# Kernel tuning notes

Measured on AMD Instinct MI355X. Metric: run time of the kernel, lower is better.

## Reference

```python
import jax, jax.numpy as jnp
import numpy as np

TT_IN = (8, 8, 8, 8)
TT_OUT = (8, 8, 8, 8)
TT_RANKS = (1, 32, 32, 32, 1)
BATCH = 4096
N_IN = int(np.prod(TT_IN))     # 4096
N_OUT = int(np.prod(TT_OUT))   # 4096
KERNEL_LEN = int(sum(TT_RANKS[k] * TT_IN[k] * TT_OUT[k] * TT_RANKS[k + 1]
                     for k in range(len(TT_IN))))  # 135168


def setup_inputs() -> dict:
    key = jax.random.key(0)
    kx, kk = jax.random.split(key)
    x = jax.random.normal(kx, (BATCH, N_IN), dtype=jnp.float32)
    # flat packed TT cores (the layer stores all cores in one 1-D weight)
    kernel = 0.02 * jax.random.normal(kk, (KERNEL_LEN,), dtype=jnp.float32)
    bias = jnp.zeros((N_OUT,), dtype=jnp.float32)
    return {"x": x, "kernel": kernel, "bias": bias}


def reference(x, kernel, bias):
    # Faithful translation of TensorTrainDense.call: iterate cores k = d-1 .. 0,
    # slicing the flat kernel from index 0 (matching the original code exactly).
    batch = x.shape[0]
    res = x
    idx = 0
    for k in range(len(TT_IN) - 1, -1, -1):
        m = TT_IN[k] * TT_RANKS[k + 1]   # contraction dim
        n = TT_RANKS[k] * TT_OUT[k]      # output dim of this core
        core = kernel[idx:idx + m * n].reshape(m, n)
        res = res.reshape(-1, m) @ core              # (-1, r_k*out_k)
        res = res.reshape(-1, TT_OUT[k]).T           # (out_k, -1)
        idx += m * n
    res = res.reshape(-1, batch).T                   # (batch, prod(out))
    return res + bias
```

## Files before the change

### kernel.cpp

```cpp
#include <hip/hip_runtime.h>
#include <hip/hip_bf16.h>

typedef unsigned short u16;
typedef __attribute__((ext_vector_type(8))) short  bf16x8;
typedef __attribute__((ext_vector_type(4))) float  fx4;

#define OFF_C0 0
#define OFF_C1 2048
#define OFF_C2 67584
#define OFF_C3 133120

static __device__ __forceinline__ u16 f2bf(float f) {
  union { __hip_bfloat16 h; u16 u; } cv;
  cv.h = __float2bfloat16(f);
  return cv.u;
}
static __device__ __forceinline__ float bf2f(u16 u) {
  union { u16 u; __hip_bfloat16 h; } cv;
  cv.u = u;
  return __bfloat162float(cv.h);
}

__global__ void build_w34T(const float* __restrict__ ker, float* __restrict__ w34T) {
  int t = blockIdx.x * 256 + threadIdx.x;
  int i34 = t & 63, c = t >> 6;
  int a2 = c >> 6, o3 = (c >> 3) & 7, o4 = c & 7;
  int i3 = i34 >> 3, i4 = i34 & 7;
  float s = 0.f;
#pragma unroll 8
  for (int a3 = 0; a3 < 32; ++a3) {
    float k1 = ker[OFF_C1 + (i3 * 32 + a3) * 256 + a2 * 8 + o3];
    float k0 = ker[OFF_C0 + i4 * 256 + a3 * 8 + o4];
    s += k1 * k0;
  }
  w34T[c * 64 + i34] = s;
}

__global__ void build_w234t2(const float* __restrict__ ker, const float* __restrict__ w34T,
                             u16* __restrict__ w234t) {
  int t = blockIdx.x * 256 + threadIdx.x;
  int i234 = t & 511, g = t >> 9;
  int a1 = g >> 3, o3 = g & 7;
  int i2 = i234 >> 6, i34 = i234 & 63;
  float acc[8][8];
#pragma unroll
  for (int a = 0; a < 8; ++a)
#pragma unroll
    for (int b = 0; b < 8; ++b) acc[a][b] = 0.f;
  for (int a2 = 0; a2 < 32; ++a2) {
    float w[8];
#pragma unroll
    for (int o4 = 0; o4 < 8; ++o4)
      w[o4] = w34T[(a2 * 64 + o3 * 8 + o4) * 64 + i34];
#pragma unroll
    for (int o2 = 0; o2 < 8; ++o2) {
      float c2 = ker[OFF_C2 + (i2 * 32 + a2) * 256 + a1 * 8 + o2];
#pragma unroll
      for (int o4 = 0; o4 < 8; ++o4) acc[o2][o4] += c2 * w[o4];
    }
  }
#pragma unroll
  for (int o2 = 0; o2 < 8; ++o2) {
    int cg = a1 * 64 + o2 * 8 + o3;
#pragma unroll
    for (int o4 = 0; o4 < 8; ++o4)
      w234t[(cg * 8 + o4) * 512 + i234] = f2bf(acc[o2][o4]);
  }
}

__global__ void build_wt2(const float* __restrict__ ker, const u16* __restrict__ w234t,
                          u16* __restrict__ wt) {
  int t = blockIdx.x * 256 + threadIdx.x;
  int i234 = t & 511, j234 = t >> 9;
  float acc[8][8];
#pragma unroll
  for (int a = 0; a < 8; ++a)
#pragma unroll
    for (int b = 0; b < 8; ++b) acc[a][b] = 0.f;
  for (int a1 = 0; a1 < 32; ++a1) {
    float w = bf2f(w234t[(a1 * 512 + j234) * 512 + i234]);
#pragma unroll
    for (int i1 = 0; i1 < 8; ++i1) {
      const float* c3 = ker + OFF_C3 + (i1 * 32 + a1) * 8;
#pragma unroll
      for (int o1 = 0; o1 < 8; ++o1) acc[i1][o1] += c3[o1] * w;
    }
  }
#pragma unroll
  for (int o1 = 0; o1 < 8; ++o1)
#pragma unroll
    for (int i1 = 0; i1 < 8; ++i1)
      wt[(size_t)(o1 * 512 + j234) * 4096 + i1 * 512 + i234] = f2bf(acc[i1][o1]);
}

__global__ void x_to_bf16(const float* __restrict__ x, u16* __restrict__ xb) {
  int t = blockIdx.x * 256 + threadIdx.x;
  const fx4* p = (const fx4*)(x + (size_t)t * 8);
  fx4 v0 = p[0], v1 = p[1];
  u16 tmp[8];
#pragma unroll
  for (int q = 0; q < 4; ++q) tmp[q] = f2bf(v0[q]);
#pragma unroll
  for (int q = 0; q < 4; ++q) tmp[4 + q] = f2bf(v1[q]);
  typedef __attribute__((ext_vector_type(8))) u16 u16x8;
  *(u16x8*)(xb + (size_t)t * 8) = *(const u16x8*)tmp;
}

__device__ __forceinline__ void gld16(const u16* g, u16* l) {
  __builtin_amdgcn_global_load_lds((const __attribute__((address_space(1))) void*)g,
                                   (__attribute__((address_space(3))) void*)l, 16, 0, 0);
}

__global__ __launch_bounds__(512, 2) void gemm_bt4(const u16* __restrict__ A, const u16* __restrict__ Bt,
                                                   const float* __restrict__ bias, float* __restrict__ C) {
  __shared__ __align__(16) u16 sh[65536];

  const int tid = threadIdx.x;
  const int lane = tid & 63;
  const int wave = tid >> 6;
  const int wm = wave >> 2, wn = wave & 3;
  const int fr = lane & 15, fg = lane >> 4;

  const int bid = blockIdx.x;
  const int wg = (bid & 7) * 32 + (bid >> 3);
  const int bm = (wg >> 4) * 256, bn = (wg & 15) * 256;

  const int srow = tid >> 2;
  const int sco = (((tid & 3) ^ ((tid >> 3) & 3)) * 8);
  const size_t agA0 = (size_t)(bm + srow) * 4096 + sco;
  const size_t agA1 = agA0 + (size_t)128 * 4096;
  const size_t agB0 = (size_t)(bn + srow) * 4096 + sco;
  const size_t agB1 = agB0 + (size_t)128 * 4096;
  const int ldsW = wave * 512;

  fx4 acc[8][4];
#pragma unroll
  for (int m = 0; m < 8; ++m)
#pragma unroll
    for (int n = 0; n < 4; ++n) acc[m][n] = (fx4){0.f, 0.f, 0.f, 0.f};

  for (int pt = 0; pt < 3; ++pt) {
    u16* Aq = sh + pt * 8192;
    u16* Bq = sh + 32768 + pt * 8192;
    gld16(A + agA0 + pt * 32, Aq + ldsW);
    gld16(A + agA1 + pt * 32, Aq + ldsW + 4096);
    gld16(Bt + agB0 + pt * 32, Bq + ldsW);
    gld16(Bt + agB1 + pt * 32, Bq + ldsW + 4096);
  }
  asm volatile("s_waitcnt vmcnt(8)" ::: "memory");
  __builtin_amdgcn_s_barrier();

  for (int t = 0; t < 128; ++t) {
    u16* Ap = sh + (t & 3) * 8192;
    u16* Bp = sh + 32768 + (t & 3) * 8192;
    u16* Aq = sh + ((t + 3) & 3) * 8192;
    u16* Bq = sh + 32768 + ((t + 3) & 3) * 8192;
    const size_t ko = (size_t)(((t + 3) & 127) * 32);

    bf16x8 av[4], bv[4], aw[4];
#pragma unroll
    for (int m = 0; m < 4; ++m) {
      const int R = wm * 128 + m * 16 + fr;
      av[m] = *(const bf16x8*)(Ap + R * 32 + ((fg ^ ((R >> 1) & 3)) * 8));
    }
#pragma unroll
    for (int n = 0; n < 4; ++n) {
      const int R = wn * 64 + n * 16 + fr;
      bv[n] = *(const bf16x8*)(Bp + R * 32 + ((fg ^ ((R >> 1) & 3)) * 8));
    }
#pragma unroll
    for (int m = 0; m < 4; ++m) {
      const int R = wm * 128 + 64 + m * 16 + fr;
      aw[m] = *(const bf16x8*)(Ap + R * 32 + ((fg ^ ((R >> 1) & 3)) * 8));
    }

    gld16(A + agA0 + ko, Aq + ldsW);
    gld16(A + agA1 + ko, Aq + ldsW + 4096);
    gld16(Bt + agB0 + ko, Bq + ldsW);
    gld16(Bt + agB1 + ko, Bq + ldsW + 4096);

    __builtin_amdgcn_s_setprio(1);
#pragma unroll
    for (int m = 0; m < 4; ++m)
#pragma unroll
      for (int n = 0; n < 4; ++n)
        acc[m][n] = __builtin_amdgcn_mfma_f32_16x16x32_bf16(av[m], bv[n], acc[m][n], 0, 0, 0);
#pragma unroll
    for (int m = 0; m < 4; ++m)
#pragma unroll
      for (int n = 0; n < 4; ++n)
        acc[4 + m][n] = __builtin_amdgcn_mfma_f32_16x16x32_bf16(aw[m], bv[n], acc[4 + m][n], 0, 0, 0);
    __builtin_amdgcn_s_setprio(0);

    asm volatile("s_waitcnt vmcnt(8)" ::: "memory");
    __builtin_amdgcn_s_barrier();
  }

  const int crow0 = bm + wm * 128 + fg * 4;
  const int ccol0 = bn + wn * 64 + fr;
#pragma unroll
  for (int n = 0; n < 4; ++n) {
    const int col = ccol0 + n * 16;
    const float bvl = bias[col];
#pragma unroll
    for (int mf = 0; mf < 8; ++mf) {
      const int r0 = crow0 + mf * 16;
#pragma unroll
      for (int q = 0; q < 4; ++q)
        C[(size_t)(r0 + q) * 4096 + col] = acc[mf][n][q] + bvl;
    }
  }
}

extern "C" void kernel_launch(void* const* d_in, const int* in_sizes, int n_in,
                              void* d_out, int out_size, void* d_ws, size_t ws_size,
                              hipStream_t stream) {
  const float* x    = (const float*)d_in[0];
  const float* ker  = (const float*)d_in[1];
  const float* bias = (const float*)d_in[2];
  float* out = (float*)d_out;

  char* ws = (char*)d_ws;
  u16*  xb    = (u16*)ws;
  u16*  wt    = (u16*)(ws + 33554432);
  u16*  w234t = (u16*)(ws + 67108864);
  float* w34T = (float*)(ws + 83886080);

  x_to_bf16   <<<8192, 256, 0, stream>>>(x, xb);
  build_w34T  <<<512, 256, 0, stream>>>(ker, w34T);
  build_w234t2<<<512, 256, 0, stream>>>(ker, w34T, w234t);
  build_wt2   <<<1024, 256, 0, stream>>>(ker, w234t, wt);
  gemm_bt4    <<<256, 512, 0, stream>>>(xb, wt, bias, out);
}
```

Measured before the change: 177.5 us.

## Fuse x conversion with w34T build and retile GEMM to 128x256 blocks

```diff
diff --git a/kernel.cpp b/kernel.cpp
--- a/kernel.cpp
+++ b/kernel.cpp
@@ -21,19 +21,33 @@
   return __bfloat162float(cv.h);
 }
 
-__global__ void build_w34T(const float* __restrict__ ker, float* __restrict__ w34T) {
-  int t = blockIdx.x * 256 + threadIdx.x;
-  int i34 = t & 63, c = t >> 6;
-  int a2 = c >> 6, o3 = (c >> 3) & 7, o4 = c & 7;
-  int i3 = i34 >> 3, i4 = i34 & 7;
-  float s = 0.f;
+__global__ void x_and_w34T(const float* __restrict__ x, u16* __restrict__ xb,
+                           const float* __restrict__ ker, float* __restrict__ w34T) {
+  if (blockIdx.x < 8192) {
+    int t = blockIdx.x * 256 + threadIdx.x;
+    const fx4* p = (const fx4*)(x + (size_t)t * 8);
+    fx4 v0 = p[0], v1 = p[1];
+    u16 tmp[8];
+#pragma unroll
+    for (int q = 0; q < 4; ++q) tmp[q] = f2bf(v0[q]);
+#pragma unroll
+    for (int q = 0; q < 4; ++q) tmp[4 + q] = f2bf(v1[q]);
+    typedef __attribute__((ext_vector_type(8))) u16 u16x8;
+    *(u16x8*)(xb + (size_t)t * 8) = *(const u16x8*)tmp;
+  } else {
+    int t = (blockIdx.x - 8192) * 256 + threadIdx.x;
+    int i34 = t & 63, c = t >> 6;
+    int a2 = c >> 6, o3 = (c >> 3) & 7, o4 = c & 7;
+    int i3 = i34 >> 3, i4 = i34 & 7;
+    float s = 0.f;
 #pragma unroll 8
-  for (int a3 = 0; a3 < 32; ++a3) {
-    float k1 = ker[OFF_C1 + (i3 * 32 + a3) * 256 + a2 * 8 + o3];
-    float k0 = ker[OFF_C0 + i4 * 256 + a3 * 8 + o4];
-    s += k1 * k0;
-  }
-  w34T[c * 64 + i34] = s;
+    for (int a3 = 0; a3 < 32; ++a3) {
+      float k1 = ker[OFF_C1 + (i3 * 32 + a3) * 256 + a2 * 8 + o3];
+      float k0 = ker[OFF_C0 + i4 * 256 + a3 * 8 + o4];
+      s += k1 * k0;
+    }
+    w34T[c * 64 + i34] = s;
+  }
 }
 
 __global__ void build_w234t2(const float* __restrict__ ker, const float* __restrict__ w34T,
@@ -93,123 +107,114 @@
       wt[(size_t)(o1 * 512 + j234) * 4096 + i1 * 512 + i234] = f2bf(acc[i1][o1]);
 }
 
-__global__ void x_to_bf16(const float* __restrict__ x, u16* __restrict__ xb) {
-  int t = blockIdx.x * 256 + threadIdx.x;
-  const fx4* p = (const fx4*)(x + (size_t)t * 8);
-  fx4 v0 = p[0], v1 = p[1];
-  u16 tmp[8];
-#pragma unroll
-  for (int q = 0; q < 4; ++q) tmp[q] = f2bf(v0[q]);
-#pragma unroll
-  for (int q = 0; q < 4; ++q) tmp[4 + q] = f2bf(v1[q]);
-  typedef __attribute__((ext_vector_type(8))) u16 u16x8;
-  *(u16x8*)(xb + (size_t)t * 8) = *(const u16x8*)tmp;
-}
-
 __device__ __forceinline__ void gld16(const u16* g, u16* l) {
   __builtin_amdgcn_global_load_lds((const __attribute__((address_space(1))) void*)g,
                                    (__attribute__((address_space(3))) void*)l, 16, 0, 0);
 }
 
-__global__ __launch_bounds__(512, 2) void gemm_bt4(const u16* __restrict__ A, const u16* __restrict__ Bt,
-                                                   const float* __restrict__ bias, float* __restrict__ C) {
-  __shared__ __align__(16) u16 sh[65536];
+__global__ __launch_bounds__(256, 2) void gemm_half(const u16* __restrict__ A, const u16* __restrict__ Bt,
+                                                    const float* __restrict__ bias, float* __restrict__ C) {
+  __shared__ __align__(16) u16 sh[36864];
 
   const int tid = threadIdx.x;
   const int lane = tid & 63;
   const int wave = tid >> 6;
-  const int wm = wave >> 2, wn = wave & 3;
+  const int wm = wave >> 1, wn = wave & 1;
   const int fr = lane & 15, fg = lane >> 4;
 
   const int bid = blockIdx.x;
-  const int wg = (bid & 7) * 32 + (bid >> 3);
-  const int bm = (wg >> 4) * 256, bn = (wg & 15) * 256;
-
-  const int srow = tid >> 2;
-  const int sco = (((tid & 3) ^ ((tid >> 3) & 3)) * 8);
-  const size_t agA0 = (size_t)(bm + srow) * 4096 + sco;
-  const size_t agA1 = agA0 + (size_t)128 * 4096;
-  const size_t agB0 = (size_t)(bn + srow) * 4096 + sco;
-  const size_t agB1 = agB0 + (size_t)128 * 4096;
-  const int ldsW = wave * 512;
-
-  fx4 acc[8][4];
-#pragma unroll
-  for (int m = 0; m < 8; ++m)
-#pragma unroll
-    for (int n = 0; n < 4; ++n) acc[m][n] = (fx4){0.f, 0.f, 0.f, 0.f};
-
-  for (int pt = 0; pt < 3; ++pt) {
-    u16* Aq = sh + pt * 8192;
-    u16* Bq = sh + 32768 + pt * 8192;
-    gld16(A + agA0 + pt * 32, Aq + ldsW);
-    gld16(A + agA1 + pt * 32, Aq + ldsW + 4096);
-    gld16(Bt + agB0 + pt * 32, Bq + ldsW);
-    gld16(Bt + agB1 + pt * 32, Bq + ldsW + 4096);
-  }
-  asm volatile("s_waitcnt vmcnt(8)" ::: "memory");
+  const int wg = (bid & 7) * 64 + (bid >> 3);
+  const int bm = (wg >> 4) * 128, bn = (wg & 15) * 256;
+
+  const int lq = lane >> 2, ls = lane & 3;
+  size_t agA[2], agB[4];
+#pragma unroll
+  for (int L = 0; L < 2; ++L) {
+    const int row = (wave * 2 + L) * 16 + lq;
+    agA[L] = (size_t)(bm + row) * 4096 + ((ls ^ ((row >> 1) & 3)) * 8);
+  }
+#pragma unroll
+  for (int L = 0; L < 4; ++L) {
+    const int row = (wave * 4 + L) * 16 + lq;
+    agB[L] = (size_t)(bn + row) * 4096 + ((ls ^ ((row >> 1) & 3)) * 8);
+  }
+  u16* const ldA0 = sh + (wave * 2) * 512;
+  u16* const ldB0 = sh + 12288 + (wave * 4) * 512;
+
+  int aoff[4], boff[8];
+#pragma unroll
+  for (int m = 0; m < 4; ++m) {
+    const int R = wm * 64 + m * 16 + fr;
+    aoff[m] = R * 32 + ((fg ^ ((R >> 1) & 3)) * 8);
+  }
+#pragma unroll
+  for (int n = 0; n < 8; ++n) {
+    const int R = wn * 128 + n * 16 + fr;
+    boff[n] = R * 32 + ((fg ^ ((R >> 1) & 3)) * 8);
+  }
+
+  fx4 acc[4][8];
+#pragma unroll
+  for (int m = 0; m < 4; ++m)
+#pragma unroll
+    for (int n = 0; n < 8; ++n) acc[m][n] = (fx4){0.f, 0.f, 0.f, 0.f};
+
+#define STAGE(buf, t) do { const size_t k_ = (size_t)(((t) & 127) * 32); \
+    u16* a_ = ldA0 + (buf) * 4096; u16* b_ = ldB0 + (buf) * 8192; \
+    gld16(A + agA[0] + k_, a_); \
+    gld16(A + agA[1] + k_, a_ + 512); \
+    gld16(Bt + agB[0] + k_, b_); \
+    gld16(Bt + agB[1] + k_, b_ + 512); \
+    gld16(Bt + agB[2] + k_, b_ + 1024); \
+    gld16(Bt + agB[3] + k_, b_ + 1536); } while (0)
+
+  STAGE(0, 0);
+  STAGE(1, 1);
+  asm volatile("s_waitcnt vmcnt(6)" ::: "memory");
   __builtin_amdgcn_s_barrier();
 
+  int p = 0;
   for (int t = 0; t < 128; ++t) {
-    u16* Ap = sh + (t & 3) * 8192;
-    u16* Bp = sh + 32768 + (t & 3) * 8192;
-    u16* Aq = sh + ((t + 3) & 3) * 8192;
-    u16* Bq = sh + 32768 + ((t + 3) & 3) * 8192;
-    const size_t ko = (size_t)(((t + 3) & 127) * 32);
-
-    bf16x8 av[4], bv[4], aw[4];
-#pragma unroll
-    for (int m = 0; m < 4; ++m) {
-      const int R = wm * 128 + m * 16 + fr;
-      av[m] = *(const bf16x8*)(Ap + R * 32 + ((fg ^ ((R >> 1) & 3)) * 8));
-    }
-#pragma unroll
-    for (int n = 0; n < 4; ++n) {
-      const int R = wn * 64 + n * 16 + fr;
-      bv[n] = *(const bf16x8*)(Bp + R * 32 + ((fg ^ ((R >> 1) & 3)) * 8));
-    }
-#pragma unroll
-    for (int m = 0; m < 4; ++m) {
-      const int R = wm * 128 + 64 + m * 16 + fr;
-      aw[m] = *(const bf16x8*)(Ap + R * 32 + ((fg ^ ((R >> 1) & 3)) * 8));
-    }
-
-    gld16(A + agA0 + ko, Aq + ldsW);
-    gld16(A + agA1 + ko, Aq + ldsW + 4096);
-    gld16(Bt + agB0 + ko, Bq + ldsW);
-    gld16(Bt + agB1 + ko, Bq + ldsW + 4096);
+    const int ps = p + 2 >= 3 ? p - 1 : p + 2;
+    const u16* Ap = sh + p * 4096;
+    const u16* Bp = sh + 12288 + p * 8192;
+
+    bf16x8 av[4], bv[8];
+#pragma unroll
+    for (int m = 0; m < 4; ++m) av[m] = *(const bf16x8*)(Ap + aoff[m]);
+#pragma unroll
+    for (int n = 0; n < 8; ++n) bv[n] = *(const bf16x8*)(Bp + boff[n]);
+
+    STAGE(ps, t + 2);
 
     __builtin_amdgcn_s_setprio(1);
 #pragma unroll
     for (int m = 0; m < 4; ++m)
 #pragma unroll
-      for (int n = 0; n < 4; ++n)
+      for (int n = 0; n < 8; ++n)
         acc[m][n] = __builtin_amdgcn_mfma_f32_16x16x32_bf16(av[m], bv[n], acc[m][n], 0, 0, 0);
-#pragma unroll
-    for (int m = 0; m < 4; ++m)
-#pragma unroll
-      for (int n = 0; n < 4; ++n)
-        acc[4 + m][n] = __builtin_amdgcn_mfma_f32_16x16x32_bf16(aw[m], bv[n], acc[4 + m][n], 0, 0, 0);
     __builtin_amdgcn_s_setprio(0);
 
-    asm volatile("s_waitcnt vmcnt(8)" ::: "memory");
+    asm volatile("s_waitcnt vmcnt(6)" ::: "memory");
     __builtin_amdgcn_s_barrier();
-  }
-
-  const int crow0 = bm + wm * 128 + fg * 4;
-  const int ccol0 = bn + wn * 64 + fr;
-#pragma unroll
-  for (int n = 0; n < 4; ++n) {
+    p = p + 1 >= 3 ? 0 : p + 1;
+  }
+
+  const int crow0 = bm + wm * 64 + fg * 4;
+  const int ccol0 = bn + wn * 128 + fr;
+#pragma unroll
+  for (int n = 0; n < 8; ++n) {
     const int col = ccol0 + n * 16;
     const float bvl = bias[col];
 #pragma unroll
-    for (int mf = 0; mf < 8; ++mf) {
-      const int r0 = crow0 + mf * 16;
+    for (int m = 0; m < 4; ++m) {
+      const int r0 = crow0 + m * 16;
 #pragma unroll
       for (int q = 0; q < 4; ++q)
-        C[(size_t)(r0 + q) * 4096 + col] = acc[mf][n][q] + bvl;
-    }
-  }
+        C[(size_t)(r0 + q) * 4096 + col] = acc[m][n][q] + bvl;
+    }
+  }
+#undef STAGE
 }
 
 extern "C" void kernel_launch(void* const* d_in, const int* in_sizes, int n_in,
@@ -226,9 +231,8 @@
   u16*  w234t = (u16*)(ws + 67108864);
   float* w34T = (float*)(ws + 83886080);
 
-  x_to_bf16   <<<8192, 256, 0, stream>>>(x, xb);
-  build_w34T  <<<512, 256, 0, stream>>>(ker, w34T);
+  x_and_w34T  <<<8704, 256, 0, stream>>>(x, xb, ker, w34T);
   build_w234t2<<<512, 256, 0, stream>>>(ker, w34T, w234t);
   build_wt2   <<<1024, 256, 0, stream>>>(ker, w234t, wt);
-  gemm_bt4    <<<256, 512, 0, stream>>>(xb, wt, bias, out);
-}
+  gemm_half   <<<512, 256, 0, stream>>>(xb, wt, bias, out);
+}
```

Result: slower. 211.2 us (+19.0%).

## Pre-swizzle weight into MFMA fragment layout and load B directly to registers

Applied to the files above, without the earlier changes.

```diff
diff --git a/kernel.cpp b/kernel.cpp
--- a/kernel.cpp
+++ b/kernel.cpp
@@ -3,6 +3,7 @@
 
 typedef unsigned short u16;
 typedef __attribute__((ext_vector_type(8))) short  bf16x8;
+typedef __attribute__((ext_vector_type(8))) u16    u16x8;
 typedef __attribute__((ext_vector_type(4))) float  fx4;
 
 #define OFF_C0 0
@@ -21,19 +22,32 @@
   return __bfloat162float(cv.h);
 }
 
-__global__ void build_w34T(const float* __restrict__ ker, float* __restrict__ w34T) {
-  int t = blockIdx.x * 256 + threadIdx.x;
-  int i34 = t & 63, c = t >> 6;
-  int a2 = c >> 6, o3 = (c >> 3) & 7, o4 = c & 7;
-  int i3 = i34 >> 3, i4 = i34 & 7;
-  float s = 0.f;
+__global__ void x_and_w34T(const float* __restrict__ x, u16* __restrict__ xb,
+                           const float* __restrict__ ker, float* __restrict__ w34T) {
+  if (blockIdx.x < 8192) {
+    int t = blockIdx.x * 256 + threadIdx.x;
+    const fx4* p = (const fx4*)(x + (size_t)t * 8);
+    fx4 v0 = p[0], v1 = p[1];
+    u16 tmp[8];
+#pragma unroll
+    for (int q = 0; q < 4; ++q) tmp[q] = f2bf(v0[q]);
+#pragma unroll
+    for (int q = 0; q < 4; ++q) tmp[4 + q] = f2bf(v1[q]);
+    *(u16x8*)(xb + (size_t)t * 8) = *(const u16x8*)tmp;
+  } else {
+    int t = (blockIdx.x - 8192) * 256 + threadIdx.x;
+    int i34 = t & 63, c = t >> 6;
+    int a2 = c >> 6, o3 = (c >> 3) & 7, o4 = c & 7;
+    int i3 = i34 >> 3, i4 = i34 & 7;
+    float s = 0.f;
 #pragma unroll 8
-  for (int a3 = 0; a3 < 32; ++a3) {
-    float k1 = ker[OFF_C1 + (i3 * 32 + a3) * 256 + a2 * 8 + o3];
-    float k0 = ker[OFF_C0 + i4 * 256 + a3 * 8 + o4];
-    s += k1 * k0;
-  }
-  w34T[c * 64 + i34] = s;
+    for (int a3 = 0; a3 < 32; ++a3) {
+      float k1 = ker[OFF_C1 + (i3 * 32 + a3) * 256 + a2 * 8 + o3];
+      float k0 = ker[OFF_C0 + i4 * 256 + a3 * 8 + o4];
+      s += k1 * k0;
+    }
+    w34T[c * 64 + i34] = s;
+  }
 }
 
 __global__ void build_w234t2(const float* __restrict__ ker, const float* __restrict__ w34T,
@@ -68,8 +82,8 @@
   }
 }
 
-__global__ void build_wt2(const float* __restrict__ ker, const u16* __restrict__ w234t,
-                          u16* __restrict__ wt) {
+__global__ void build_wt4(const float* __restrict__ ker, const u16* __restrict__ w234t,
+                          u16* __restrict__ wtt) {
   int t = blockIdx.x * 256 + threadIdx.x;
   int i234 = t & 511, j234 = t >> 9;
   float acc[8][8];
@@ -86,24 +100,18 @@
       for (int o1 = 0; o1 < 8; ++o1) acc[i1][o1] += c3[o1] * w;
     }
   }
-#pragma unroll
-  for (int o1 = 0; o1 < 8; ++o1)
-#pragma unroll
-    for (int i1 = 0; i1 < 8; ++i1)
-      wt[(size_t)(o1 * 512 + j234) * 4096 + i1 * 512 + i234] = f2bf(acc[i1][o1]);
-}
-
-__global__ void x_to_bf16(const float* __restrict__ x, u16* __restrict__ xb) {
-  int t = blockIdx.x * 256 + threadIdx.x;
-  const fx4* p = (const fx4*)(x + (size_t)t * 8);
-  fx4 v0 = p[0], v1 = p[1];
-  u16 tmp[8];
-#pragma unroll
-  for (int q = 0; q < 4; ++q) tmp[q] = f2bf(v0[q]);
-#pragma unroll
-  for (int q = 0; q < 4; ++q) tmp[4 + q] = f2bf(v1[q]);
-  typedef __attribute__((ext_vector_type(8))) u16 u16x8;
-  *(u16x8*)(xb + (size_t)t * 8) = *(const u16x8*)tmp;
+  const int e    = i234 & 7;
+  const int l    = (j234 & 15) | (((i234 >> 3) & 3) << 4);
+  const int kklo = i234 >> 5;
+#pragma unroll
+  for (int o1 = 0; o1 < 8; ++o1) {
+    const int n16 = o1 * 32 + (j234 >> 4);
+#pragma unroll
+    for (int i1 = 0; i1 < 8; ++i1) {
+      const int kk = i1 * 16 + kklo;
+      wtt[((size_t)kk * 256 + n16) * 512 + l * 8 + e] = f2bf(acc[i1][o1]);
+    }
+  }
 }
 
 __device__ __forceinline__ void gld16(const u16* g, u16* l) {
@@ -111,9 +119,9 @@
                                    (__attribute__((address_space(3))) void*)l, 16, 0, 0);
 }
 
-__global__ __launch_bounds__(512, 2) void gemm_bt4(const u16* __restrict__ A, const u16* __restrict__ Bt,
-                                                   const float* __restrict__ bias, float* __restrict__ C) {
-  __shared__ __align__(16) u16 sh[65536];
+__global__ __launch_bounds__(512, 2) void gemm_bdir(const u16* __restrict__ A, const u16* __restrict__ Bg,
+                                                    const float* __restrict__ bias, float* __restrict__ C) {
+  __shared__ __align__(16) u16 sh[32768];
 
   const int tid = threadIdx.x;
   const int lane = tid & 63;
@@ -129,71 +137,61 @@
   const int sco = (((tid & 3) ^ ((tid >> 3) & 3)) * 8);
   const size_t agA0 = (size_t)(bm + srow) * 4096 + sco;
   const size_t agA1 = agA0 + (size_t)128 * 4096;
-  const size_t agB0 = (size_t)(bn + srow) * 4096 + sco;
-  const size_t agB1 = agB0 + (size_t)128 * 4096;
   const int ldsW = wave * 512;
 
+  int aoff[8];
+#pragma unroll
+  for (int m = 0; m < 8; ++m) {
+    const int R = wm * 128 + m * 16 + fr;
+    aoff[m] = R * 32 + ((fg ^ ((R >> 1) & 3)) * 8);
+  }
+
+  const u16* const Bw = Bg + ((size_t)((bn >> 4) + wn * 4)) * 512 + lane * 8;
+
   fx4 acc[8][4];
 #pragma unroll
   for (int m = 0; m < 8; ++m)
 #pragma unroll
     for (int n = 0; n < 4; ++n) acc[m][n] = (fx4){0.f, 0.f, 0.f, 0.f};
 
-  for (int pt = 0; pt < 3; ++pt) {
-    u16* Aq = sh + pt * 8192;
-    u16* Bq = sh + 32768 + pt * 8192;
-    gld16(A + agA0 + pt * 32, Aq + ldsW);
-    gld16(A + agA1 + pt * 32, Aq + ldsW + 4096);
-    gld16(Bt + agB0 + pt * 32, Bq + ldsW);
-    gld16(Bt + agB1 + pt * 32, Bq + ldsW + 4096);
-  }
-  asm volatile("s_waitcnt vmcnt(8)" ::: "memory");
+#define STAGE_A(buf, tt) do { const size_t ko = (size_t)((tt) & 127) * 32; \
+    u16* a_ = sh + (buf) * 8192 + ldsW; \
+    gld16(A + agA0 + ko, a_); \
+    gld16(A + agA1 + ko, a_ + 4096); } while (0)
+#define LOADB(dst, tt) do { const size_t bo = (size_t)((tt) & 127) * 131072; \
+    _Pragma("unroll") \
+    for (int n_ = 0; n_ < 4; ++n_) dst[n_] = *(const bf16x8*)(Bw + bo + n_ * 512); } while (0)
+
+  bf16x8 bva[4], bvb[4];
+
+  LOADB(bva, 0);
+  STAGE_A(0, 0);
+  STAGE_A(1, 1);
+  STAGE_A(2, 2);
+  asm volatile("s_waitcnt vmcnt(4)" ::: "memory");
   __builtin_amdgcn_s_barrier();
 
-  for (int t = 0; t < 128; ++t) {
-    u16* Ap = sh + (t & 3) * 8192;
-    u16* Bp = sh + 32768 + (t & 3) * 8192;
-    u16* Aq = sh + ((t + 3) & 3) * 8192;
-    u16* Bq = sh + 32768 + ((t + 3) & 3) * 8192;
-    const size_t ko = (size_t)(((t + 3) & 127) * 32);
-
-    bf16x8 av[4], bv[4], aw[4];
-#pragma unroll
-    for (int m = 0; m < 4; ++m) {
-      const int R = wm * 128 + m * 16 + fr;
-      av[m] = *(const bf16x8*)(Ap + R * 32 + ((fg ^ ((R >> 1) & 3)) * 8));
-    }
-#pragma unroll
-    for (int n = 0; n < 4; ++n) {
-      const int R = wn * 64 + n * 16 + fr;
-      bv[n] = *(const bf16x8*)(Bp + R * 32 + ((fg ^ ((R >> 1) & 3)) * 8));
-    }
-#pragma unroll
-    for (int m = 0; m < 4; ++m) {
-      const int R = wm * 128 + 64 + m * 16 + fr;
-      aw[m] = *(const bf16x8*)(Ap + R * 32 + ((fg ^ ((R >> 1) & 3)) * 8));
-    }
-
-    gld16(A + agA0 + ko, Aq + ldsW);
-    gld16(A + agA1 + ko, Aq + ldsW + 4096);
-    gld16(Bt + agB0 + ko, Bq + ldsW);
-    gld16(Bt + agB1 + ko, Bq + ldsW + 4096);
-
-    __builtin_amdgcn_s_setprio(1);
-#pragma unroll
-    for (int m = 0; m < 4; ++m)
-#pragma unroll
-      for (int n = 0; n < 4; ++n)
-        acc[m][n] = __builtin_amdgcn_mfma_f32_16x16x32_bf16(av[m], bv[n], acc[m][n], 0, 0, 0);
-#pragma unroll
-    for (int m = 0; m < 4; ++m)
-#pragma unroll
-      for (int n = 0; n < 4; ++n)
-        acc[4 + m][n] = __builtin_amdgcn_mfma_f32_16x16x32_bf16(aw[m], bv[n], acc[4 + m][n], 0, 0, 0);
-    __builtin_amdgcn_s_setprio(0);
-
-    asm volatile("s_waitcnt vmcnt(8)" ::: "memory");
-    __builtin_amdgcn_s_barrier();
+#define BODY(t, bvc, bvn) do { \
+    const u16* Ap = sh + ((t) & 3) * 8192; \
+    LOADB(bvn, (t) + 1); \
+    bf16x8 av[8]; \
+    _Pragma("unroll") \
+    for (int m_ = 0; m_ < 8; ++m_) av[m_] = *(const bf16x8*)(Ap + aoff[m_]); \
+    STAGE_A(((t) + 3) & 3, (t) + 3); \
+    __builtin_amdgcn_s_setprio(1); \
+    _Pragma("unroll") \
+    for (int m_ = 0; m_ < 8; ++m_) \
+      _Pragma("unroll") \
+      for (int n_ = 0; n_ < 4; ++n_) \
+        acc[m_][n_] = __builtin_amdgcn_mfma_f32_16x16x32_bf16(av[m_], bvc[n_], acc[m_][n_], 0, 0, 0); \
+    __builtin_amdgcn_s_setprio(0); \
+    asm volatile("s_waitcnt vmcnt(8)" ::: "memory"); \
+    __builtin_amdgcn_s_barrier(); \
+  } while (0)
+
+  for (int t = 0; t < 128; t += 2) {
+    BODY(t, bva, bvb);
+    BODY(t + 1, bvb, bva);
   }
 
   const int crow0 = bm + wm * 128 + fg * 4;
@@ -210,6 +208,9 @@
         C[(size_t)(r0 + q) * 4096 + col] = acc[mf][n][q] + bvl;
     }
   }
+#undef STAGE_A
+#undef LOADB
+#undef BODY
 }
 
 extern "C" void kernel_launch(void* const* d_in, const int* in_sizes, int n_in,
@@ -222,13 +223,12 @@
 
   char* ws = (char*)d_ws;
   u16*  xb    = (u16*)ws;
-  u16*  wt    = (u16*)(ws + 33554432);
+  u16*  wtt   = (u16*)(ws + 33554432);
   u16*  w234t = (u16*)(ws + 67108864);
   float* w34T = (float*)(ws + 83886080);
 
-  x_to_bf16   <<<8192, 256, 0, stream>>>(x, xb);
-  build_w34T  <<<512, 256, 0, stream>>>(ker, w34T);
+  x_and_w34T  <<<8704, 256, 0, stream>>>(x, xb, ker, w34T);
   build_w234t2<<<512, 256, 0, stream>>>(ker, w34T, w234t);
-  build_wt2   <<<1024, 256, 0, stream>>>(ker, w234t, wt);
-  gemm_bt4    <<<256, 512, 0, stream>>>(xb, wt, bias, out);
-}
+  build_wt4   <<<1024, 256, 0, stream>>>(ker, w234t, wtt);
+  gemm_bdir   <<<256, 512, 0, stream>>>(xb, wtt, bias, out);
+}
```

Result: slower. 210.6 us (+18.6%).

## Fuse fp32-to-bf16 conversion of x into GEMM loads, drop x_to_bf16 kernel

Applied to the files above, without the earlier changes.

```diff
diff --git a/kernel.cpp b/kernel.cpp
--- a/kernel.cpp
+++ b/kernel.cpp
@@ -3,6 +3,7 @@
 
 typedef unsigned short u16;
 typedef __attribute__((ext_vector_type(8))) short  bf16x8;
+typedef __attribute__((ext_vector_type(8))) u16    u16x8;
 typedef __attribute__((ext_vector_type(4))) float  fx4;
 
 #define OFF_C0 0
@@ -93,27 +94,15 @@
       wt[(size_t)(o1 * 512 + j234) * 4096 + i1 * 512 + i234] = f2bf(acc[i1][o1]);
 }
 
-__global__ void x_to_bf16(const float* __restrict__ x, u16* __restrict__ xb) {
-  int t = blockIdx.x * 256 + threadIdx.x;
-  const fx4* p = (const fx4*)(x + (size_t)t * 8);
-  fx4 v0 = p[0], v1 = p[1];
-  u16 tmp[8];
-#pragma unroll
-  for (int q = 0; q < 4; ++q) tmp[q] = f2bf(v0[q]);
-#pragma unroll
-  for (int q = 0; q < 4; ++q) tmp[4 + q] = f2bf(v1[q]);
-  typedef __attribute__((ext_vector_type(8))) u16 u16x8;
-  *(u16x8*)(xb + (size_t)t * 8) = *(const u16x8*)tmp;
-}
-
-__device__ __forceinline__ void gld16(const u16* g, u16* l) {
+__device__ __forceinline__ void gld16(const void* g, void* l) {
   __builtin_amdgcn_global_load_lds((const __attribute__((address_space(1))) void*)g,
                                    (__attribute__((address_space(3))) void*)l, 16, 0, 0);
 }
 
-__global__ __launch_bounds__(512, 2) void gemm_bt4(const u16* __restrict__ A, const u16* __restrict__ Bt,
-                                                   const float* __restrict__ bias, float* __restrict__ C) {
-  __shared__ __align__(16) u16 sh[65536];
+__global__ __launch_bounds__(512, 2) void gemm_f32a(const float* __restrict__ X, const u16* __restrict__ Bt,
+                                                    const float* __restrict__ bias, float* __restrict__ C) {
+  __shared__ __align__(16) float shA[24576];
+  __shared__ __align__(16) u16   shB[24576];
 
   const int tid = threadIdx.x;
   const int lane = tid & 63;
@@ -125,13 +114,34 @@
   const int wg = (bid & 7) * 32 + (bid >> 3);
   const int bm = (wg >> 4) * 256, bn = (wg & 15) * 256;
 
-  const int srow = tid >> 2;
-  const int sco = (((tid & 3) ^ ((tid >> 3) & 3)) * 8);
-  const size_t agA0 = (size_t)(bm + srow) * 4096 + sco;
-  const size_t agA1 = agA0 + (size_t)128 * 4096;
-  const size_t agB0 = (size_t)(bn + srow) * 4096 + sco;
-  const size_t agB1 = agB0 + (size_t)128 * 4096;
-  const int ldsW = wave * 512;
+  size_t agA[4];
+#pragma unroll
+  for (int L = 0; L < 4; ++L) {
+    const int r = L * 64 + (tid >> 3);
+    agA[L] = (size_t)(bm + r) * 4096 + (((tid & 7) ^ (r & 7)) * 4);
+  }
+  size_t agB[2];
+#pragma unroll
+  for (int L = 0; L < 2; ++L) {
+    const int r = L * 128 + (tid >> 2);
+    agB[L] = (size_t)(bn + r) * 4096 + (((tid & 3) ^ ((r >> 1) & 3)) * 8);
+  }
+  const int ldsWA = wave * 256;
+  const int ldsWB = wave * 512;
+
+  int aoff[8][2], boff[4];
+#pragma unroll
+  for (int m = 0; m < 8; ++m) {
+    const int R = wm * 128 + m * 16 + fr;
+#pragma unroll
+    for (int h = 0; h < 2; ++h)
+      aoff[m][h] = R * 32 + (((fg * 2 + h) ^ (R & 7)) * 4);
+  }
+#pragma unroll
+  for (int n = 0; n < 4; ++n) {
+    const int R = wn * 64 + n * 16 + fr;
+    boff[n] = R * 32 + ((fg ^ ((R >> 1) & 3)) * 8);
+  }
 
   fx4 acc[8][4];
 #pragma unroll
@@ -139,61 +149,56 @@
 #pragma unroll
     for (int n = 0; n < 4; ++n) acc[m][n] = (fx4){0.f, 0.f, 0.f, 0.f};
 
-  for (int pt = 0; pt < 3; ++pt) {
-    u16* Aq = sh + pt * 8192;
-    u16* Bq = sh + 32768 + pt * 8192;
-    gld16(A + agA0 + pt * 32, Aq + ldsW);
-    gld16(A + agA1 + pt * 32, Aq + ldsW + 4096);
-    gld16(Bt + agB0 + pt * 32, Bq + ldsW);
-    gld16(Bt + agB1 + pt * 32, Bq + ldsW + 4096);
-  }
-  asm volatile("s_waitcnt vmcnt(8)" ::: "memory");
+#define STAGE(buf, tt) do { const int k_ = ((tt) & 127) * 32; \
+    float* a_ = shA + (buf) * 8192 + ldsWA; u16* b_ = shB + (buf) * 8192 + ldsWB; \
+    gld16(X + agA[0] + k_, a_); \
+    gld16(X + agA[1] + k_, a_ + 2048); \
+    gld16(X + agA[2] + k_, a_ + 4096); \
+    gld16(X + agA[3] + k_, a_ + 6144); \
+    gld16(Bt + agB[0] + k_, b_); \
+    gld16(Bt + agB[1] + k_, b_ + 4096); } while (0)
+
+  STAGE(0, 0);
+  STAGE(1, 1);
+  asm volatile("s_waitcnt vmcnt(6)" ::: "memory");
   __builtin_amdgcn_s_barrier();
 
+  int p = 0;
   for (int t = 0; t < 128; ++t) {
-    u16* Ap = sh + (t & 3) * 8192;
-    u16* Bp = sh + 32768 + (t & 3) * 8192;
-    u16* Aq = sh + ((t + 3) & 3) * 8192;
-    u16* Bq = sh + 32768 + ((t + 3) & 3) * 8192;
-    const size_t ko = (size_t)(((t + 3) & 127) * 32);
-
-    bf16x8 av[4], bv[4], aw[4];
-#pragma unroll
-    for (int m = 0; m < 4; ++m) {
-      const int R = wm * 128 + m * 16 + fr;
-      av[m] = *(const bf16x8*)(Ap + R * 32 + ((fg ^ ((R >> 1) & 3)) * 8));
-    }
-#pragma unroll
-    for (int n = 0; n < 4; ++n) {
-      const int R = wn * 64 + n * 16 + fr;
-      bv[n] = *(const bf16x8*)(Bp + R * 32 + ((fg ^ ((R >> 1) & 3)) * 8));
-    }
-#pragma unroll
-    for (int m = 0; m < 4; ++m) {
-      const int R = wm * 128 + 64 + m * 16 + fr;
-      aw[m] = *(const bf16x8*)(Ap + R * 32 + ((fg ^ ((R >> 1) & 3)) * 8));
-    }
-
-    gld16(A + agA0 + ko, Aq + ldsW);
-    gld16(A + agA1 + ko, Aq + ldsW + 4096);
-    gld16(Bt + agB0 + ko, Bq + ldsW);
-    gld16(Bt + agB1 + ko, Bq + ldsW + 4096);
+    const int ps = p + 2 >= 3 ? p - 1 : p + 2;
+    const float* Ap = shA + p * 8192;
+    const u16*   Bp = shB + p * 8192;
+
+    bf16x8 bv[4];
+#pragma unroll
+    for (int n = 0; n < 4; ++n) bv[n] = *(const bf16x8*)(Bp + boff[n]);
+
+    bf16x8 av[8];
+#pragma unroll
+    for (int m = 0; m < 8; ++m) {
+      fx4 lo = *(const fx4*)(Ap + aoff[m][0]);
+      fx4 hi = *(const fx4*)(Ap + aoff[m][1]);
+      u16 tmp[8];
+#pragma unroll
+      for (int q = 0; q < 4; ++q) tmp[q] = f2bf(lo[q]);
+#pragma unroll
+      for (int q = 0; q < 4; ++q) tmp[4 + q] = f2bf(hi[q]);
+      av[m] = *(const bf16x8*)tmp;
+    }
+
+    STAGE(ps, t + 2);
 
     __builtin_amdgcn_s_setprio(1);
 #pragma unroll
-    for (int m = 0; m < 4; ++m)
+    for (int m = 0; m < 8; ++m)
 #pragma unroll
       for (int n = 0; n < 4; ++n)
         acc[m][n] = __builtin_amdgcn_mfma_f32_16x16x32_bf16(av[m], bv[n], acc[m][n], 0, 0, 0);
-#pragma unroll
-    for (int m = 0; m < 4; ++m)
-#pragma unroll
-      for (int n = 0; n < 4; ++n)
-        acc[4 + m][n] = __builtin_amdgcn_mfma_f32_16x16x32_bf16(aw[m], bv[n], acc[4 + m][n], 0, 0, 0);
     __builtin_amdgcn_s_setprio(0);
 
-    asm volatile("s_waitcnt vmcnt(8)" ::: "memory");
+    asm volatile("s_waitcnt vmcnt(6)" ::: "memory");
     __builtin_amdgcn_s_barrier();
+    p = p + 1 >= 3 ? 0 : p + 1;
   }
 
   const int crow0 = bm + wm * 128 + fg * 4;
@@ -210,6 +215,7 @@
         C[(size_t)(r0 + q) * 4096 + col] = acc[mf][n][q] + bvl;
     }
   }
+#undef STAGE
 }
 
 extern "C" void kernel_launch(void* const* d_in, const int* in_sizes, int n_in,
@@ -221,14 +227,12 @@
   float* out = (float*)d_out;
 
   char* ws = (char*)d_ws;
-  u16*  xb    = (u16*)ws;
-  u16*  wt    = (u16*)(ws + 33554432);
-  u16*  w234t = (u16*)(ws + 67108864);
-  float* w34T = (float*)(ws + 83886080);
-
-  x_to_bf16   <<<8192, 256, 0, stream>>>(x, xb);
+  u16*  wt    = (u16*)ws;
+  u16*  w234t = (u16*)(ws + 33554432);
+  float* w34T = (float*)(ws + 50331648);
+
   build_w34T  <<<512, 256, 0, stream>>>(ker, w34T);
   build_w234t2<<<512, 256, 0, stream>>>(ker, w34T, w234t);
   build_wt2   <<<1024, 256, 0, stream>>>(ker, w234t, wt);
-  gemm_bt4    <<<256, 512, 0, stream>>>(xb, wt, bias, out);
-}
+  gemm_f32a   <<<256, 512, 0, stream>>>(x, wt, bias, out);
+}
```

New measurement: 192.2 us. 1.08x slower.
